# Performance work log

Measured on AMD Instinct MI355X. Metric: run time of the kernel, lower is better.

Reference implementation:

```python
import jax, jax.numpy as jnp
import numpy as np

N_E = 1024
E_DIM = 256
TAU = 0.5
BETA = 0.25
LAMB = 0.1
EPS = 1e-10


def setup_inputs() -> dict:
    key = jax.random.key(0)
    k1, k2, k3 = jax.random.split(key, 3)
    z = jax.random.normal(k1, (16, 1024, E_DIM), dtype=jnp.float32)
    # kaiming-normal-initialized codebook (std = sqrt(2 / fan_in))
    emb = jax.random.normal(k2, (N_E, E_DIM), dtype=jnp.float32) * np.sqrt(2.0 / E_DIM)
    u = jax.random.uniform(k3, (16 * 1024, N_E), dtype=jnp.float32)
    return {"z": z, "emb": emb, "u": u}


def reference(z, emb, u):
    zf = z.reshape(-1, E_DIM)                                  # [N, e_dim]
    # squared euclidean distances to each code: ||z||^2 + ||e||^2 - 2 z.e
    d = (jnp.sum(zf * zf, axis=1, keepdims=True)
         + jnp.sum(emb * emb, axis=1)
         - 2.0 * jnp.matmul(zf, emb.T))                        # [N, n_e]
    # gumbel-softmax (hard, straight-through) on logits = -d
    g = -jnp.log(-jnp.log(u + EPS) + EPS)
    y_soft = jax.nn.softmax((-d + g) / TAU, axis=-1)
    idx = jnp.argmax(y_soft, axis=-1)
    y_hard = jax.nn.one_hot(idx, N_E, dtype=y_soft.dtype)
    probs = y_hard + y_soft - jax.lax.stop_gradient(y_soft)    # [N, n_e]
    z_q = jnp.matmul(probs, emb).reshape(z.shape)
    # orthogonality loss on the codebook gram matrix
    gram = jnp.matmul(emb, emb.T)
    ortho = jnp.mean((gram - jnp.eye(N_E, dtype=emb.dtype)) ** 2) / (N_E ** 2)
    emb_loss = jnp.mean((jax.lax.stop_gradient(z_q) - z) ** 2)
    commit = BETA * jnp.mean((z_q - jax.lax.stop_gradient(z)) ** 2)
    loss = emb_loss + BETA * commit + LAMB * ortho
    z_q_st = z + jax.lax.stop_gradient(z_q - z)
    e_mean = jnp.mean(probs, axis=0)
    perplexity = jnp.exp(-jnp.sum(e_mean * jnp.log(e_mean + EPS)))
    return loss, z_q_st, perplexity
```

## Files before the change

### kernel.cpp

```cpp
#include <hip/hip_runtime.h>
#include <math.h>
#include <stdint.h>


#define NROWS 16384
#define NE    1024
#define ED    256
#define EPSF  1e-10f
#define INV2048 4.8828125e-4f
#define BK 64
#define BM 128
#define BN 64
#define SCW 68

typedef _Float16 half_t;
typedef __attribute__((ext_vector_type(4))) _Float16 half4;
typedef __attribute__((ext_vector_type(8))) _Float16 half8;
typedef __attribute__((ext_vector_type(16))) float floatx16;
typedef unsigned long long u64;

__device__ __forceinline__ void gl_lds16(const half_t* g, half_t* l) {
    __builtin_amdgcn_global_load_lds(
        (const __attribute__((address_space(1))) uint32_t*)g,
        (__attribute__((address_space(3))) uint32_t*)l, 16, 0, 0);
}

__device__ __forceinline__ u64 packMax(float v, int code) {
    unsigned int b   = __float_as_uint(v);
    unsigned int key = (b & 0x80000000u) ? ~b : (b | 0x80000000u);
    return ((u64)key << 32) | (unsigned int)(NE - 1 - code);
}

__global__ __launch_bounds__(256) void vq_prep(
        const float* __restrict__ z, const float* __restrict__ emb,
        half_t* __restrict__ zh, half_t* __restrict__ zl,
        half_t* __restrict__ eh, half_t* __restrict__ el,
        float* __restrict__ enorm, float* __restrict__ znorm,
        u64* __restrict__ best, int* __restrict__ cnt,
        double* __restrict__ mse_acc, int* __restrict__ done_cnt)
{
    const int gid = blockIdx.x * 256 + threadIdx.x;
    const int ZQ4 = NROWS * ED / 4;
    if (gid < ZQ4) {
        const float4 v = ((const float4*)z)[gid];
        const float x[4] = {v.x, v.y, v.z, v.w};
        half4 h, l;
#pragma unroll
        for (int i = 0; i < 4; ++i) {
            const half_t hi = (half_t)x[i];
            h[i] = hi; l[i] = (half_t)((x[i] - (float)hi) * 2048.0f);
        }
        *(half4*)&zh[(size_t)gid * 4] = h;
        *(half4*)&zl[(size_t)gid * 4] = l;
        float s = v.x*v.x + v.y*v.y + v.z*v.z + v.w*v.w;
#pragma unroll
        for (int o = 32; o; o >>= 1) s += __shfl_down(s, o);
        if ((threadIdx.x & 63) == 0) znorm[gid >> 6] = s;
    } else {
        const int eg = gid - ZQ4;
        const float4 v = ((const float4*)emb)[eg];
        const float x[4] = {v.x, v.y, v.z, v.w};
        half4 h, l;
#pragma unroll
        for (int i = 0; i < 4; ++i) {
            const half_t hi = (half_t)x[i];
            h[i] = hi; l[i] = (half_t)((x[i] - (float)hi) * 2048.0f);
        }
        *(half4*)&eh[(size_t)eg * 4] = h;
        *(half4*)&el[(size_t)eg * 4] = l;
        float s = v.x*v.x + v.y*v.y + v.z*v.z + v.w*v.w;
#pragma unroll
        for (int o = 32; o; o >>= 1) s += __shfl_down(s, o);
        if ((threadIdx.x & 63) == 0) enorm[eg >> 6] = s;
        if (eg < NROWS) best[eg] = 0ull;
        if (eg < NE)    cnt[eg]  = 0;
        if (eg == 0)  { *mse_acc = 0.0; *done_cnt = 0; }
    }
}

__global__ __launch_bounds__(256, 3) void vq_gemm(
        const half_t* __restrict__ zh, const half_t* __restrict__ zl,
        const half_t* __restrict__ eh, const half_t* __restrict__ el,
        const float* __restrict__ u, const float* __restrict__ enorm,
        u64* __restrict__ best)
{
    __shared__ __align__(16) char smem[51200];
    half_t* Ah = (half_t*)smem;
    half_t* Al = (half_t*)(smem + 16384);
    half_t* Bh = (half_t*)(smem + 32768);
    half_t* Bl = (half_t*)(smem + 40960);
    float (*Sc)[SCW] = (float(*)[SCW])smem;
    u64* parr = (u64*)(smem + 49152);

    const int t    = threadIdx.x;
    const int w    = t >> 6;
    const int lane = t & 63;
    const int lrow = lane & 31;
    const int hw   = lane >> 5;
    const int m0 = blockIdx.x * BM, n0 = blockIdx.y * BN;
    const int wm = (w >> 1) * 64, wn = (w & 1) * 32;

    size_t gaoff[4], gboff[2];
#pragma unroll
    for (int it = 0; it < 4; ++it) {
        const int s = it * 256 + t;
        const int row = s >> 3;
        const int c = (s & 7) ^ (row & 7);
        gaoff[it] = (size_t)(m0 + row) * ED + c * 8;
    }
#pragma unroll
    for (int it = 0; it < 2; ++it) {
        const int s = it * 256 + t;
        const int row = s >> 3;
        const int c = (s & 7) ^ (row & 7);
        gboff[it] = (size_t)(n0 + row) * ED + c * 8;
    }

    floatx16 accH[2] = {};
    floatx16 accX[2] = {};

    for (int kc = 0; kc < ED; kc += BK) {
        __syncthreads();
#pragma unroll
        for (int it = 0; it < 4; ++it) {
            const int ldsoff = (it * 256 + w * 64) * 8;
            gl_lds16(zh + gaoff[it] + kc, Ah + ldsoff);
            gl_lds16(zl + gaoff[it] + kc, Al + ldsoff);
        }
#pragma unroll
        for (int it = 0; it < 2; ++it) {
            const int ldsoff = (it * 256 + w * 64) * 8;
            gl_lds16(eh + gboff[it] + kc, Bh + ldsoff);
            gl_lds16(el + gboff[it] + kc, Bl + ldsoff);
        }
        __syncthreads();
#pragma unroll
        for (int ks = 0; ks < BK / 16; ++ks) {
            const int cch = ks * 2 + hw;
            const int br = wn + lrow;
            const int sb = br * 8 + (cch ^ (br & 7));
            const half8 bh = *(const half8*)&Bh[sb * 8];
            const half8 bl = *(const half8*)&Bl[sb * 8];
            half8 ah[2], al[2];
#pragma unroll
            for (int i = 0; i < 2; ++i) {
                const int ar = wm + i * 32 + lrow;
                const int sa = ar * 8 + (cch ^ (ar & 7));
                ah[i] = *(const half8*)&Ah[sa * 8];
                al[i] = *(const half8*)&Al[sa * 8];
            }
#pragma unroll
            for (int i = 0; i < 2; ++i) {
                accH[i] = __builtin_amdgcn_mfma_f32_32x32x16_f16(ah[i], bh, accH[i], 0, 0, 0);
                accX[i] = __builtin_amdgcn_mfma_f32_32x32x16_f16(ah[i], bl, accX[i], 0, 0, 0);
                accX[i] = __builtin_amdgcn_mfma_f32_32x32x16_f16(al[i], bh, accX[i], 0, 0, 0);
            }
        }
    }
    __syncthreads();

    const int   col0 = n0 + wn + lrow;
    const float en0  = enorm[col0];
#pragma unroll
    for (int i = 0; i < 2; ++i) {
#pragma unroll
        for (int r = 0; r < 16; ++r) {
            const int lr = wm + i * 32 + (r & 3) + ((r >> 2) << 3) + (hw << 2);
            const float d  = accH[i][r] + accX[i][r] * INV2048;
            const float uv = u[(size_t)(m0 + lr) * NE + col0];
            const float g  = -__logf(-__logf(uv + EPSF) + EPSF);
            Sc[lr][wn + lrow] = 2.f * d - en0 + g;
        }
    }
    __syncthreads();

    {
        const int row = t >> 1;
        const int ch  = (t & 1) << 5;
        float bv = -1e38f; int bc = 0;
#pragma unroll
        for (int q = 0; q < 8; ++q) {
            const float4 v = *(const float4*)&Sc[row][ch + (q << 2)];
            const int c = n0 + ch + (q << 2);
            if (v.x > bv) { bv = v.x; bc = c; }
            if (v.y > bv) { bv = v.y; bc = c + 1; }
            if (v.z > bv) { bv = v.z; bc = c + 2; }
            if (v.w > bv) { bv = v.w; bc = c + 3; }
        }
        parr[t] = packMax(bv, bc);
    }
    __syncthreads();
    if (t < 128) {
        const u64 a = parr[t << 1], b = parr[(t << 1) + 1];
        atomicMax(&best[m0 + t], a > b ? a : b);
    }
}

__global__ __launch_bounds__(256) void vq_outfin(
        const float* __restrict__ emb, const float* __restrict__ u,
        const u64* __restrict__ best, const float* __restrict__ znorm,
        int* __restrict__ cnt, double* __restrict__ mse_acc,
        int* __restrict__ done_cnt, float* __restrict__ out)
{
    __shared__ int    ridx[64];
    __shared__ double redd[4];
    __shared__ int    flag;
    const int t  = threadIdx.x;
    const int m0 = blockIdx.x * 64;

    if (t < 64) {
        const u64 p = best[m0 + t];
        const unsigned int key = (unsigned int)(p >> 32);
        const int code = NE - 1 - (int)(p & 0xFFFFFFFFu);
        ridx[t] = code;
        atomicAdd(&cnt[code], 1);
        const unsigned int b = (key & 0x80000000u) ? (key ^ 0x80000000u) : ~key;
        const float s  = __uint_as_float(b);
        const float uv = u[(size_t)(m0 + t) * NE + code];
        const float g  = -__logf(-__logf(uv + EPSF) + EPSF);
        float lm = znorm[m0 + t] - s + g;
#pragma unroll
        for (int o = 32; o; o >>= 1) lm += __shfl_down(lm, o);
        if (t == 0) atomicAdd(mse_acc, (double)lm);
    }
    __syncthreads();

    const int wv = t >> 6, l = t & 63;
#pragma unroll
    for (int rr = 0; rr < 16; ++rr) {
        const int row = (rr << 2) + wv;
        const int j   = ridx[row];
        const size_t ob = 1 + (size_t)(m0 + row) * ED;
        const size_t eb = (size_t)j * ED;
#pragma unroll
        for (int q = 0; q < 4; ++q) {
            const int c = (q << 6) + l;
            out[ob + c] = emb[eb + c];
        }
    }

    if (t == 0) {
        __threadfence();
        flag = (atomicAdd(done_cnt, 1) == NROWS / 64 - 1) ? 1 : 0;
    }
    __syncthreads();
    if (flag) {
        double s = 0.0;
#pragma unroll
        for (int q = 0; q < 4; ++q) {
            const int   c  = atomicAdd(&cnt[(q << 8) + t], 0);
            const float em = (float)c / (float)NROWS;
            s += (double)(em * logf(em + EPSF));
        }
#pragma unroll
        for (int o = 32; o; o >>= 1) s += __shfl_down(s, o);
        if ((t & 63) == 0) redd[t >> 6] = s;
        __syncthreads();
        if (t == 0) {
            const double tot = redd[0] + redd[1] + redd[2] + redd[3];
            const double mse = atomicAdd(mse_acc, 0.0) / (double)((size_t)NROWS * ED);
            out[0] = (float)(mse * 1.0625);
            out[1 + (size_t)NROWS * ED] = (float)exp(-tot);
        }
    }
}

extern "C" void kernel_launch(void* const* d_in, const int* in_sizes, int n_in,
                              void* d_out, int out_size, void* d_ws, size_t ws_size,
                              hipStream_t stream) {
    const float* z   = (const float*)d_in[0];
    const float* emb = (const float*)d_in[1];
    const float* u   = (const float*)d_in[2];
    float* out = (float*)d_out;

    double* mse_acc  = (double*)d_ws;
    int*    done_cnt = (int*)((char*)d_ws + 64);
    int*    cnt      = (int*)((char*)d_ws + 1024);
    float*  enorm    = (float*)((char*)d_ws + 5120);
    u64*    best     = (u64*)((char*)d_ws + 9216);
    float*  znorm    = (float*)((char*)d_ws + 140288);
    const size_t small_end = 205824;

    const size_t zsplit = (size_t)NROWS * ED * 2;
    const size_t esplit = (size_t)NE * ED * 2;
    const bool bigws = ws_size >= small_end + 2 * zsplit + 2 * esplit;

    half_t *zh, *zl, *eh, *el;
    if (bigws) {
        char* big = (char*)d_ws + small_end;
        zh = (half_t*)big;
        zl = (half_t*)(big + zsplit);
        eh = (half_t*)(big + 2 * zsplit);
        el = (half_t*)(big + 2 * zsplit + esplit);
    } else {
        zh = (half_t*)((char*)d_out + 8);
        zl = (half_t*)((char*)d_out + 8 + zsplit);
        eh = (half_t*)((char*)d_ws + small_end);
        el = (half_t*)((char*)d_ws + small_end + esplit);
    }

    vq_prep<<<(NROWS * ED / 4 + NE * ED / 4) / 256, 256, 0, stream>>>(
        z, emb, zh, zl, eh, el, enorm, znorm, best, cnt, mse_acc, done_cnt);
    vq_gemm<<<dim3(NROWS / BM, NE / BN), 256, 0, stream>>>(
        zh, zl, eh, el, u, enorm, best);
    vq_outfin<<<NROWS / 64, 256, 0, stream>>>(
        emb, u, best, znorm, cnt, mse_acc, done_cnt, out);
}
```

Baseline: 174.7 us.

## Stage gumbel noise tile via LDS, remap blocks per XCD, restructure K-loop sync

The GEMM kernel now copies the 128x64 tile of uniform noise into a dedicated LDS region with async global-to-LDS loads, instead of each thread doing strided scalar global reads in the epilogue. It also switches to a 1D grid with an XCD-aware block mapping so that blocks on the same XCD share z row-blocks and stay within one L2. The K loop is rearranged to issue the next stage's loads after the compute barrier, removing the separate leading barrier. LDS grows to about 68 KB and launch bounds drop from 3 to 2 blocks per CU, which lowers occupancy in exchange for coalesced noise loads and better cache locality.

```diff
diff --git a/kernel.cpp b/kernel.cpp
--- a/kernel.cpp
+++ b/kernel.cpp
@@ -19,7 +19,7 @@
 typedef __attribute__((ext_vector_type(16))) float floatx16;
 typedef unsigned long long u64;
 
-__device__ __forceinline__ void gl_lds16(const half_t* g, half_t* l) {
+__device__ __forceinline__ void gl_lds16(const void* g, void* l) {
     __builtin_amdgcn_global_load_lds(
         (const __attribute__((address_space(1))) uint32_t*)g,
         (__attribute__((address_space(3))) uint32_t*)l, 16, 0, 0);
@@ -78,26 +78,31 @@
     }
 }
 
-__global__ __launch_bounds__(256, 3) void vq_gemm(
+__global__ __launch_bounds__(256, 2) void vq_gemm(
         const half_t* __restrict__ zh, const half_t* __restrict__ zl,
         const half_t* __restrict__ eh, const half_t* __restrict__ el,
         const float* __restrict__ u, const float* __restrict__ enorm,
         u64* __restrict__ best)
 {
-    __shared__ __align__(16) char smem[51200];
+    __shared__ __align__(16) char smem[69632];
     half_t* Ah = (half_t*)smem;
     half_t* Al = (half_t*)(smem + 16384);
     half_t* Bh = (half_t*)(smem + 32768);
     half_t* Bl = (half_t*)(smem + 40960);
-    float (*Sc)[SCW] = (float(*)[SCW])smem;
-    u64* parr = (u64*)(smem + 49152);
+    float*  Uf = (float*)smem;
+    float (*Sc)[SCW] = (float(*)[SCW])(smem + 32768);
+    u64* parr = (u64*)(smem + 67584);
 
     const int t    = threadIdx.x;
     const int w    = t >> 6;
     const int lane = t & 63;
     const int lrow = lane & 31;
     const int hw   = lane >> 5;
-    const int m0 = blockIdx.x * BM, n0 = blockIdx.y * BN;
+
+    const int bid = blockIdx.x;
+    const int xcd = bid & 7, c = bid >> 3;
+    const int m0 = (xcd * 16 + (c >> 4)) * BM;
+    const int n0 = (c & 15) * BN;
     const int wm = (w >> 1) * 64, wn = (w & 1) * 32;
 
     size_t gaoff[4], gboff[2];
@@ -105,22 +110,18 @@
     for (int it = 0; it < 4; ++it) {
         const int s = it * 256 + t;
         const int row = s >> 3;
-        const int c = (s & 7) ^ (row & 7);
-        gaoff[it] = (size_t)(m0 + row) * ED + c * 8;
+        const int cc = (s & 7) ^ (row & 7);
+        gaoff[it] = (size_t)(m0 + row) * ED + cc * 8;
     }
 #pragma unroll
     for (int it = 0; it < 2; ++it) {
         const int s = it * 256 + t;
         const int row = s >> 3;
-        const int c = (s & 7) ^ (row & 7);
-        gboff[it] = (size_t)(n0 + row) * ED + c * 8;
-    }
-
-    floatx16 accH[2] = {};
-    floatx16 accX[2] = {};
-
-    for (int kc = 0; kc < ED; kc += BK) {
-        __syncthreads();
+        const int cc = (s & 7) ^ (row & 7);
+        gboff[it] = (size_t)(n0 + row) * ED + cc * 8;
+    }
+
+    auto STAGE = [&](int kc) {
 #pragma unroll
         for (int it = 0; it < 4; ++it) {
             const int ldsoff = (it * 256 + w * 64) * 8;
@@ -133,6 +134,16 @@
             gl_lds16(eh + gboff[it] + kc, Bh + ldsoff);
             gl_lds16(el + gboff[it] + kc, Bl + ldsoff);
         }
+    };
+
+    STAGE(0);
+    const int   col0 = n0 + wn + lrow;
+    const float en0  = enorm[col0];
+
+    floatx16 accH[2] = {};
+    floatx16 accX[2] = {};
+
+    for (int kc = 0; kc < ED; kc += BK) {
         __syncthreads();
 #pragma unroll
         for (int ks = 0; ks < BK / 16; ++ks) {
@@ -156,18 +167,26 @@
                 accX[i] = __builtin_amdgcn_mfma_f32_32x32x16_f16(al[i], bh, accX[i], 0, 0, 0);
             }
         }
-    }
-    __syncthreads();
-
-    const int   col0 = n0 + wn + lrow;
-    const float en0  = enorm[col0];
+        __syncthreads();
+        if (kc + BK < ED) STAGE(kc + BK);
+    }
+
+#pragma unroll
+    for (int it = 0; it < 8; ++it) {
+        const int s = it * 256 + t;
+        const int row = s >> 4, cg = s & 15;
+        const int ldsoff = (it * 256 + w * 64) * 4;
+        gl_lds16(u + (size_t)(m0 + row) * NE + n0 + cg * 4, Uf + ldsoff);
+    }
+    __syncthreads();
+
 #pragma unroll
     for (int i = 0; i < 2; ++i) {
 #pragma unroll
         for (int r = 0; r < 16; ++r) {
             const int lr = wm + i * 32 + (r & 3) + ((r >> 2) << 3) + (hw << 2);
             const float d  = accH[i][r] + accX[i][r] * INV2048;
-            const float uv = u[(size_t)(m0 + lr) * NE + col0];
+            const float uv = Uf[lr * 64 + wn + lrow];
             const float g  = -__logf(-__logf(uv + EPSF) + EPSF);
             Sc[lr][wn + lrow] = 2.f * d - en0 + g;
         }
@@ -181,11 +200,11 @@
 #pragma unroll
         for (int q = 0; q < 8; ++q) {
             const float4 v = *(const float4*)&Sc[row][ch + (q << 2)];
-            const int c = n0 + ch + (q << 2);
-            if (v.x > bv) { bv = v.x; bc = c; }
-            if (v.y > bv) { bv = v.y; bc = c + 1; }
-            if (v.z > bv) { bv = v.z; bc = c + 2; }
-            if (v.w > bv) { bv = v.w; bc = c + 3; }
+            const int cc = n0 + ch + (q << 2);
+            if (v.x > bv) { bv = v.x; bc = cc; }
+            if (v.y > bv) { bv = v.y; bc = cc + 1; }
+            if (v.z > bv) { bv = v.z; bc = cc + 2; }
+            if (v.w > bv) { bv = v.w; bc = cc + 3; }
         }
         parr[t] = packMax(bv, bc);
     }
@@ -234,8 +253,8 @@
         const size_t eb = (size_t)j * ED;
 #pragma unroll
         for (int q = 0; q < 4; ++q) {
-            const int c = (q << 6) + l;
-            out[ob + c] = emb[eb + c];
+            const int cc = (q << 6) + l;
+            out[ob + cc] = emb[eb + cc];
         }
     }
 
@@ -248,8 +267,8 @@
         double s = 0.0;
 #pragma unroll
         for (int q = 0; q < 4; ++q) {
-            const int   c  = atomicAdd(&cnt[(q << 8) + t], 0);
-            const float em = (float)c / (float)NROWS;
+            const int   cc = atomicAdd(&cnt[(q << 8) + t], 0);
+            const float em = (float)cc / (float)NROWS;
             s += (double)(em * logf(em + EPSF));
         }
 #pragma unroll
@@ -301,7 +320,7 @@
 
     vq_prep<<<(NROWS * ED / 4 + NE * ED / 4) / 256, 256, 0, stream>>>(
         z, emb, zh, zl, eh, el, enorm, znorm, best, cnt, mse_acc, done_cnt);
-    vq_gemm<<<dim3(NROWS / BM, NE / BN), 256, 0, stream>>>(
+    vq_gemm<<<(NROWS / BM) * (NE / BN), 256, 0, stream>>>(
         zh, zl, eh, el, u, enorm, best);
     vq_outfin<<<NROWS / 64, 256, 0, stream>>>(
         emb, u, best, znorm, cnt, mse_acc, done_cnt, out);
```

Measured after the change: 172.2 us. No clear change (-1.4%).
